# Kernel optimization log

Hardware: AMD Instinct MI355X
Metric: run time of the kernel (lower is better)

Reference implementation:

```python
import jax, jax.numpy as jnp
import numpy as np

B, C, H, W = 8, 32, 256, 256


def setup_inputs() -> dict:
    key = jax.random.key(0)
    k1, k2, k3, k4 = jax.random.split(key, 4)
    shape = (B, C, H, W)
    x = jax.random.normal(k1, shape, dtype=jnp.float32)
    G1 = jax.random.normal(k2, shape, dtype=jnp.float32)
    G2 = jax.random.normal(k3, shape, dtype=jnp.float32)
    G3 = jax.random.normal(k4, shape, dtype=jnp.float32)
    return {"x": x, "G1": G1, "G2": G2, "G3": G3}


def _spn_forward(x, G1, G2, G3):
    # --- SpnBlock gate normalization (elementwise) ---
    sum_abs = jnp.abs(G1) + jnp.abs(G2) + jnp.abs(G3)
    sum_abs = jnp.where(sum_abs == 0, jnp.asarray(1e-6, x.dtype), sum_abs)
    mask = (sum_abs >= 1).astype(x.dtype)  # only normalize where sum(|g|) >= 1
    keep = 1.0 - mask
    G1 = keep * G1 + mask * (G1 / sum_abs)
    G2 = keep * G2 + mask * (G2 / sum_abs)
    G3 = keep * G3 + mask * (G3 / sum_abs)

    # --- GateRecurrent2dnoind (horizontal=True, reverse=False): left->right scan ---
    # h[i,j] = (1 - g1 - g2 - g3) * x[i,j] + g1*h[i-1,j-1] + g2*h[i,j-1] + g3*h[i+1,j-1]
    # Gates whose neighbor is out of range are zeroed (CUDA kernel semantics).
    Hd, Wd = x.shape[2], x.shape[3]
    row = jnp.arange(Hd)
    col_ok = (jnp.arange(Wd) > 0).astype(x.dtype)[None, None, None, :]  # no left col at j=0
    up_ok = (row > 0).astype(x.dtype)[None, None, :, None]
    dn_ok = (row < Hd - 1).astype(x.dtype)[None, None, :, None]
    g1 = G1 * col_ok * up_ok
    g2 = G2 * col_ok
    g3 = G3 * col_ok * dn_ok

    # move scan axis (W) to front: [W, B, C, H]
    xs = jnp.moveaxis(x, 3, 0)
    g1s = jnp.moveaxis(g1, 3, 0)
    g2s = jnp.moveaxis(g2, 3, 0)
    g3s = jnp.moveaxis(g3, 3, 0)

    def step(h_prev, inp):
        xj, a, b, c = inp  # each [B, C, H]
        zero = jnp.zeros_like(h_prev[..., :1])
        up = jnp.concatenate([zero, h_prev[..., :-1]], axis=-1)   # h_prev at row i-1
        dn = jnp.concatenate([h_prev[..., 1:], zero], axis=-1)    # h_prev at row i+1
        h = (1.0 - a - b - c) * xj + a * up + b * h_prev + c * dn
        return h, h

    init = jnp.zeros(x.shape[:3], dtype=x.dtype)  # [B, C, H]
    _, hs = jax.lax.scan(step, init, (xs, g1s, g2s, g3s))
    return jnp.moveaxis(hs, 0, 3)  # back to [B, C, H, W]


def reference(x, G1, G2, G3):
    return _spn_forward(x, G1, G2, G3)
```

## Files before the change

### kernel.cpp

```cpp
#include <hip/hip_runtime.h>


#define HD 256
#define WD 256
#define NS 32
#define STG 260
#define ARR_F (8 * STG)
#define STAGE_F (4 * ARR_F)
#define TILE_OFF (3 * STAGE_F)

#define F4E(v, e) ((e) == 0 ? (v).x : (e) == 1 ? (v).y : (e) == 2 ? (v).z : (v).w)

#define FENCE_BAR()                                      \
  do {                                                   \
    asm volatile("s_waitcnt lgkmcnt(0)" ::: "memory");   \
    __builtin_amdgcn_s_barrier();                        \
    asm volatile("" ::: "memory");                       \
  } while (0)

__global__ __launch_bounds__(320, 1) void spn_fwd(
    const float* __restrict__ x, const float* __restrict__ G1,
    const float* __restrict__ G2, const float* __restrict__ G3,
    float* __restrict__ out)
{
  __shared__ float lds_f[3 * STAGE_F + 16 * STG];

  const int tid = threadIdx.x;
  const int wid = tid >> 6;
  const int l   = tid & 63;
  const size_t pbase = (size_t)blockIdx.x * (HD * WD);
  const float* gp[4] = {x + pbase, G1 + pbase, G2 + pbase, G3 + pbase};
  float* op = out + pbase;

  if (wid < 4) {
    const int rq = l >> 2;
    const int cq = l & 3;
    const int myhalf = cq >> 1;
    float4 RA[4][4], RB[4][4];

    auto issueBlk = [&](float4 (&R)[4][4], int k) {
#pragma unroll
      for (int A = 0; A < 4; ++A)
#pragma unroll
        for (int i = 0; i < 4; ++i)
          R[A][i] = *(const float4*)(gp[A] +
              (size_t)(64 * wid + 16 * i + rq) * WD + 16 * k + 4 * cq);
    };

    auto normBlk = [&](float4 (&R)[4][4], int k) {
#pragma unroll
      for (int i = 0; i < 4; ++i) {
        const int row = 64 * wid + 16 * i + rq;
        const float uOk = (row > 0) ? 1.f : 0.f;
        const float dOk = (row < HD - 1) ? 1.f : 0.f;
        float nx[4], na[4], nb[4], nc[4];
#pragma unroll
        for (int e = 0; e < 4; ++e) {
          float a = F4E(R[1][i], e), b = F4E(R[2][i], e), c = F4E(R[3][i], e);
          float xx = F4E(R[0][i], e);
          float s = fabsf(a) + fabsf(b) + fabsf(c);
          float inv = (s >= 1.f) ? __builtin_amdgcn_rcpf(s) : 1.f;
          float cOk = (16 * k + 4 * cq + e > 0) ? 1.f : 0.f;
          float ga = a * inv * cOk * uOk;
          float gb = b * inv * cOk;
          float gc = c * inv * cOk * dOk;
          nx[e] = (1.f - ga - gb - gc) * xx;
          na[e] = ga; nb[e] = gb; nc[e] = gc;
        }
        R[0][i] = make_float4(nx[0], nx[1], nx[2], nx[3]);
        R[1][i] = make_float4(na[0], na[1], na[2], na[3]);
        R[2][i] = make_float4(nb[0], nb[1], nb[2], nb[3]);
        R[3][i] = make_float4(nc[0], nc[1], nc[2], nc[3]);
      }
    };

    auto writeHalf = [&](float4 (&R)[4][4], int hf, float* dst) {
      if (myhalf == hf) {
        const int c0 = 4 * cq - 8 * hf;
#pragma unroll
        for (int A = 0; A < 4; ++A)
#pragma unroll
          for (int i = 0; i < 4; ++i) {
            const int row = 64 * wid + 16 * i + rq;
#pragma unroll
            for (int e = 0; e < 4; ++e)
              dst[A * ARR_F + (c0 + e) * STG + row] = F4E(R[A][i], e);
          }
      }
    };

    issueBlk(RA, 0);
    issueBlk(RB, 1);
    normBlk(RA, 0);
    writeHalf(RA, 0, lds_f + 0 * STAGE_F);
    writeHalf(RA, 1, lds_f + 1 * STAGE_F);
    issueBlk(RA, 2);
    FENCE_BAR();

#pragma unroll 1
    for (int tt = 0; tt < 8; ++tt) {
      const int t0 = 4 * tt;
      const int kb = t0 / 2;
      normBlk(RB, kb + 1);
      writeHalf(RB, 0, lds_f + ((t0 + 2) % 3) * STAGE_F);
      FENCE_BAR();
      writeHalf(RB, 1, lds_f + ((t0 + 3) % 3) * STAGE_F);
      if (kb + 3 <= 15) issueBlk(RB, kb + 3);
      FENCE_BAR();
      if (kb + 2 <= 15) {
        normBlk(RA, kb + 2);
        writeHalf(RA, 0, lds_f + ((t0 + 4) % 3) * STAGE_F);
      }
      FENCE_BAR();
      if (kb + 2 <= 15) writeHalf(RA, 1, lds_f + ((t0 + 5) % 3) * STAGE_F);
      if (kb + 4 <= 15) issueBlk(RA, kb + 4);
      FENCE_BAR();
    }
  } else {
    __builtin_amdgcn_s_setprio(1);
    float h[4] = {0.f, 0.f, 0.f, 0.f};
    const int cb = 4 * (l & 3);
    const int rr = l >> 2;
    float* tile = lds_f + TILE_OFF;

    auto consume = [&](int t) {
      const float* src = lds_f + (t % 3) * STAGE_F;
      float* tl = tile + (t & 1) * (8 * STG);
#pragma unroll
      for (int c = 0; c < 8; ++c) {
        float4 d4 = *(const float4*)(src + 0 * ARR_F + c * STG + 4 * l);
        float4 a4 = *(const float4*)(src + 1 * ARR_F + c * STG + 4 * l);
        float4 b4 = *(const float4*)(src + 2 * ARR_F + c * STG + 4 * l);
        float4 c4 = *(const float4*)(src + 3 * ARR_F + c * STG + 4 * l);
        const float shU = __shfl_up(h[3], 1);
        const float shD = __shfl_down(h[0], 1);
        float hn[4];
#pragma unroll
        for (int r = 0; r < 4; ++r) {
          float up = (r == 0) ? shU : h[r - 1];
          float dn = (r == 3) ? shD : h[r + 1];
          hn[r] = fmaf(F4E(a4, r), up,
                  fmaf(F4E(b4, r), h[r],
                  fmaf(F4E(c4, r), dn, F4E(d4, r))));
        }
#pragma unroll
        for (int r = 0; r < 4; ++r) h[r] = hn[r];
        *(float4*)(tl + c * STG + 4 * l) = make_float4(hn[0], hn[1], hn[2], hn[3]);
      }
      if (t & 1) {
        const int jc = 16 * (t >> 1);
#pragma unroll
        for (int kk = 0; kk < 16; ++kk) {
          const int row = 16 * kk + rr;
          float4 o;
          o.x = tile[(cb + 0) * STG + row];
          o.y = tile[(cb + 1) * STG + row];
          o.z = tile[(cb + 2) * STG + row];
          o.w = tile[(cb + 3) * STG + row];
          *(float4*)(op + (size_t)row * WD + jc + cb) = o;
        }
      }
    };

    FENCE_BAR();

#pragma unroll 1
    for (int tt = 0; tt < 8; ++tt) {
      const int t0 = 4 * tt;
      consume(t0);     FENCE_BAR();
      consume(t0 + 1); FENCE_BAR();
      consume(t0 + 2); FENCE_BAR();
      consume(t0 + 3); FENCE_BAR();
    }
  }
}

extern "C" void kernel_launch(void* const* d_in, const int* in_sizes, int n_in,
                              void* d_out, int out_size, void* d_ws, size_t ws_size,
                              hipStream_t stream) {
  const float* x  = (const float*)d_in[0];
  const float* g1 = (const float*)d_in[1];
  const float* g2 = (const float*)d_in[2];
  const float* g3 = (const float*)d_in[3];
  float* outp = (float*)d_out;
  const int planes = out_size / (HD * WD);
  spn_fwd<<<planes, 320, 0, stream>>>(x, g1, g2, g3, outp);
}
```

Before: 98.10 us.

## Switch to double-buffered 16-column stages with register prefetch in scan warp

Replaces the triple-buffered 8-column half-stages with two 16-column LDS stages, so producers write a whole 16-column block per step and the block synchronises half as often. The consumer wave software-pipelines its LDS reads, prefetching the next column's four operands while it computes the current one, and now writes each output tile every stage. It also drops the consumer's raised priority. The cost is less slack between producer and consumer (double instead of triple buffering) and more registers held in the consumer.

```diff
diff --git a/kernel.cpp b/kernel.cpp
--- a/kernel.cpp
+++ b/kernel.cpp
@@ -3,11 +3,11 @@
 
 #define HD 256
 #define WD 256
-#define NS 32
+#define NS 16
 #define STG 260
-#define ARR_F (8 * STG)
+#define ARR_F (16 * STG)
 #define STAGE_F (4 * ARR_F)
-#define TILE_OFF (3 * STAGE_F)
+#define TILE_OFF (2 * STAGE_F)
 
 #define F4E(v, e) ((e) == 0 ? (v).x : (e) == 1 ? (v).y : (e) == 2 ? (v).z : (v).w)
 
@@ -23,7 +23,7 @@
     const float* __restrict__ G2, const float* __restrict__ G3,
     float* __restrict__ out)
 {
-  __shared__ float lds_f[3 * STAGE_F + 16 * STG];
+  __shared__ float lds_f[2 * STAGE_F + 16 * STG];
 
   const int tid = threadIdx.x;
   const int wid = tid >> 6;
@@ -35,7 +35,6 @@
   if (wid < 4) {
     const int rq = l >> 2;
     const int cq = l & 3;
-    const int myhalf = cq >> 1;
     float4 RA[4][4], RB[4][4];
 
     auto issueBlk = [&](float4 (&R)[4][4], int k) {
@@ -74,64 +73,66 @@
       }
     };
 
-    auto writeHalf = [&](float4 (&R)[4][4], int hf, float* dst) {
-      if (myhalf == hf) {
-        const int c0 = 4 * cq - 8 * hf;
+    auto writeStage = [&](float4 (&R)[4][4], float* dst) {
 #pragma unroll
-        for (int A = 0; A < 4; ++A)
+      for (int A = 0; A < 4; ++A)
 #pragma unroll
-          for (int i = 0; i < 4; ++i) {
-            const int row = 64 * wid + 16 * i + rq;
+        for (int i = 0; i < 4; ++i) {
+          const int row = 64 * wid + 16 * i + rq;
 #pragma unroll
-            for (int e = 0; e < 4; ++e)
-              dst[A * ARR_F + (c0 + e) * STG + row] = F4E(R[A][i], e);
-          }
-      }
+          for (int e = 0; e < 4; ++e)
+            dst[A * ARR_F + (4 * cq + e) * STG + row] = F4E(R[A][i], e);
+        }
     };
 
     issueBlk(RA, 0);
+    normBlk(RA, 0);
+    writeStage(RA, lds_f + 0 * STAGE_F);
     issueBlk(RB, 1);
-    normBlk(RA, 0);
-    writeHalf(RA, 0, lds_f + 0 * STAGE_F);
-    writeHalf(RA, 1, lds_f + 1 * STAGE_F);
-    issueBlk(RA, 2);
     FENCE_BAR();
 
 #pragma unroll 1
     for (int tt = 0; tt < 8; ++tt) {
-      const int t0 = 4 * tt;
-      const int kb = t0 / 2;
-      normBlk(RB, kb + 1);
-      writeHalf(RB, 0, lds_f + ((t0 + 2) % 3) * STAGE_F);
-      FENCE_BAR();
-      writeHalf(RB, 1, lds_f + ((t0 + 3) % 3) * STAGE_F);
-      if (kb + 3 <= 15) issueBlk(RB, kb + 3);
-      FENCE_BAR();
-      if (kb + 2 <= 15) {
-        normBlk(RA, kb + 2);
-        writeHalf(RA, 0, lds_f + ((t0 + 4) % 3) * STAGE_F);
+      const int t = 2 * tt;
+      if (t + 2 <= 15) issueBlk(RA, t + 2);
+      if (t + 1 <= 15) {
+        normBlk(RB, t + 1);
+        writeStage(RB, lds_f + 1 * STAGE_F);
       }
       FENCE_BAR();
-      if (kb + 2 <= 15) writeHalf(RA, 1, lds_f + ((t0 + 5) % 3) * STAGE_F);
-      if (kb + 4 <= 15) issueBlk(RA, kb + 4);
+      const int u = t + 1;
+      if (u + 2 <= 15) issueBlk(RB, u + 2);
+      if (u + 1 <= 15) {
+        normBlk(RA, u + 1);
+        writeStage(RA, lds_f + 0 * STAGE_F);
+      }
       FENCE_BAR();
     }
   } else {
-    __builtin_amdgcn_s_setprio(1);
     float h[4] = {0.f, 0.f, 0.f, 0.f};
     const int cb = 4 * (l & 3);
     const int rr = l >> 2;
     float* tile = lds_f + TILE_OFF;
 
-    auto consume = [&](int t) {
-      const float* src = lds_f + (t % 3) * STAGE_F;
-      float* tl = tile + (t & 1) * (8 * STG);
+    FENCE_BAR();
+
+#pragma unroll 1
+    for (int t = 0; t < NS; ++t) {
+      const float* src = lds_f + (t & 1) * STAGE_F;
+      float4 rd[2][4];
+
 #pragma unroll
-      for (int c = 0; c < 8; ++c) {
-        float4 d4 = *(const float4*)(src + 0 * ARR_F + c * STG + 4 * l);
-        float4 a4 = *(const float4*)(src + 1 * ARR_F + c * STG + 4 * l);
-        float4 b4 = *(const float4*)(src + 2 * ARR_F + c * STG + 4 * l);
-        float4 c4 = *(const float4*)(src + 3 * ARR_F + c * STG + 4 * l);
+      for (int A = 0; A < 4; ++A)
+        rd[0][A] = *(const float4*)(src + A * ARR_F + 0 * STG + 4 * l);
+
+#pragma unroll
+      for (int c = 0; c < 16; ++c) {
+        const int cur = c & 1, nxt = cur ^ 1;
+        if (c < 15) {
+#pragma unroll
+          for (int A = 0; A < 4; ++A)
+            rd[nxt][A] = *(const float4*)(src + A * ARR_F + (c + 1) * STG + 4 * l);
+        }
         const float shU = __shfl_up(h[3], 1);
         const float shD = __shfl_down(h[0], 1);
         float hn[4];
@@ -139,38 +140,27 @@
         for (int r = 0; r < 4; ++r) {
           float up = (r == 0) ? shU : h[r - 1];
           float dn = (r == 3) ? shD : h[r + 1];
-          hn[r] = fmaf(F4E(a4, r), up,
-                  fmaf(F4E(b4, r), h[r],
-                  fmaf(F4E(c4, r), dn, F4E(d4, r))));
+          hn[r] = fmaf(F4E(rd[cur][1], r), up,
+                  fmaf(F4E(rd[cur][2], r), h[r],
+                  fmaf(F4E(rd[cur][3], r), dn, F4E(rd[cur][0], r))));
         }
 #pragma unroll
         for (int r = 0; r < 4; ++r) h[r] = hn[r];
-        *(float4*)(tl + c * STG + 4 * l) = make_float4(hn[0], hn[1], hn[2], hn[3]);
+        *(float4*)(tile + c * STG + 4 * l) =
+            make_float4(hn[0], hn[1], hn[2], hn[3]);
       }
-      if (t & 1) {
-        const int jc = 16 * (t >> 1);
+
 #pragma unroll
-        for (int kk = 0; kk < 16; ++kk) {
-          const int row = 16 * kk + rr;
-          float4 o;
-          o.x = tile[(cb + 0) * STG + row];
-          o.y = tile[(cb + 1) * STG + row];
-          o.z = tile[(cb + 2) * STG + row];
-          o.w = tile[(cb + 3) * STG + row];
-          *(float4*)(op + (size_t)row * WD + jc + cb) = o;
-        }
+      for (int kk = 0; kk < 16; ++kk) {
+        const int row = 16 * kk + rr;
+        float4 o;
+        o.x = tile[(cb + 0) * STG + row];
+        o.y = tile[(cb + 1) * STG + row];
+        o.z = tile[(cb + 2) * STG + row];
+        o.w = tile[(cb + 3) * STG + row];
+        *(float4*)(op + (size_t)row * WD + 16 * t + cb) = o;
       }
-    };
-
-    FENCE_BAR();
-
-#pragma unroll 1
-    for (int tt = 0; tt < 8; ++tt) {
-      const int t0 = 4 * tt;
-      consume(t0);     FENCE_BAR();
-      consume(t0 + 1); FENCE_BAR();
-      consume(t0 + 2); FENCE_BAR();
-      consume(t0 + 3); FENCE_BAR();
+      FENCE_BAR();
     }
   }
 }
```

New measurement: 106.2 us. +8.2%, slower.
